# Optimization experiments

Hardware: AMD Instinct MI355X
Metric: run time of the kernel (lower is better)

The kernel has to match this reference:

```python
import jax, jax.numpy as jnp
import numpy as np

# Straight-through binarization: forward hard threshold, backward identity.
# Matches BinarizeTensorThresh / BinarizedLinearFunction / BinaryActivation STE
# semantics from the diffnaps my_layers module (grad_weight = g^T x, i.e. the
# continuous weight receives the gradient of the binary weight unchanged).

def make_ste(thresh):
    @jax.custom_vjp
    def f(x):
        return (x >= thresh).astype(x.dtype)
    def fwd(x):
        return f(x), None
    def bwd(_, g):
        return (g,)
    f.defvjp(fwd, bwd)
    return f

ste_half = make_ste(0.5)  # weight binarization threshold (the 0.5 ctor arg)
ste_one = make_ste(1.0)   # activation fires when (pre-act + bias) >= 1

B, D, H, L = 4096, 5000, 2000, 50  # batch, input_dim(items), hidden_dim(patterns), label_dim
DATA_SPARSITY = 0.05


def setup_inputs() -> dict:
    key = jax.random.key(0)
    k = jax.random.split(key, 5)
    # sparse binary transaction data
    x = (jax.random.uniform(k[0], (B, D)) < DATA_SPARSITY).astype(jnp.float32)
    # continuous encoder weight in [0,1); binarized at 0.5 inside forward
    W_enc = jax.random.uniform(k[1], (H, D), dtype=jnp.float32)
    # small negative encoder bias (BinaPs-style init)
    b_enc = -jnp.abs(jax.random.normal(k[2], (H,), dtype=jnp.float32)) * 0.1
    act0_bias = jnp.zeros((H,), jnp.float32)
    act3_bias = jnp.zeros((D,), jnp.float32)
    # classifier_weight = logit(clip(N(0.1, 0.1), 0.01, 0.99)) as in __init__
    y = jnp.clip(0.1 + 0.1 * jax.random.normal(k[3], (L, H), dtype=jnp.float32), 0.01, 0.99)
    classifier_weight = jnp.log(y / (1.0 - y))
    return {
        "x": x,
        "W_enc": W_enc,
        "b_enc": b_enc,
        "act0_bias": act0_bias,
        "act3_bias": act3_bias,
        "classifier_weight": classifier_weight,
    }


def reference(x, W_enc, b_enc, act0_bias, act3_bias, classifier_weight):
    # fc0_enc: binarized-weight linear with bias
    Wb = ste_half(W_enc)                       # [H, D] in {0,1}
    h = x @ Wb.T + b_enc                       # [B, H]
    # act0: binary activation (threshold 1 on biased pre-activation)
    z = ste_one(h + act0_bias)                 # [B, H]
    # classify: sigmoid-gated classifier head (external_classifier=None / mode 'None')
    final_w = jax.nn.sigmoid(classifier_weight / 0.5)  # [L, H]
    classification = z @ final_w.T             # [B, L]
    # fc3_dec: shares the binarized encoder weight, transposed, no bias
    xd = z @ Wb                                # [B, D]
    output = ste_one(xd + act3_bias)           # [B, D]
    return output, classification, z
```

## Files before the change

### kernel.cpp

```cpp
#include <hip/hip_runtime.h>
#include <stdint.h>

static constexpr int Bn = 4096;
static constexpr int Dn = 5000;
static constexpr int Hn = 2000;
static constexpr int Ln = 50;
static constexpr int XW = 80;
static constexpr int Hpad = 2048;
static constexpr int Dpad = 5120;

typedef int v4i __attribute__((ext_vector_type(4)));
typedef int v16i __attribute__((ext_vector_type(16)));

__device__ __forceinline__ int popc_acc(uint64_t v, int acc) {
  acc = __builtin_popcount((uint32_t)v) + acc;
  acc = __builtin_popcount((uint32_t)(v >> 32)) + acc;
  return acc;
}

__global__ void k_pack_i8(const float* __restrict__ src, uint8_t* __restrict__ dst,
                          int nrows_out, int nrows_valid, int ncols_src) {
  int g = (int)blockIdx.x * 256 + (int)threadIdx.x;
  int row = g / (Dpad / 4);
  int c4 = g - row * (Dpad / 4);
  if (row >= nrows_out) return;
  int col = c4 * 4;
  uchar4 o = make_uchar4(0, 0, 0, 0);
  if (row < nrows_valid && col + 3 < ncols_src) {
    const float4 v = *(const float4*)(src + (size_t)row * ncols_src + col);
    o.x = v.x >= 0.5f; o.y = v.y >= 0.5f; o.z = v.z >= 0.5f; o.w = v.w >= 0.5f;
  }
  *(uchar4*)(dst + (size_t)row * Dpad + col) = o;
}

__global__ void k_pack_x(const float* __restrict__ x, uint64_t* __restrict__ xb2) {
  int g = (int)((blockIdx.x * blockDim.x + threadIdx.x) >> 6);
  int lane = (int)(threadIdx.x & 63);
  constexpr int nq = XW >> 2;
  int row = g / nq;
  int q = g - row * nq;
  if (row >= Bn) return;
  int w0 = q << 2;
  unsigned long long m[4];
#pragma unroll
  for (int e = 0; e < 4; ++e) {
    int col = ((w0 + e) << 6) + lane;
    float v = (col < Dn) ? x[(size_t)row * Dn + col] : 0.0f;
    m[e] = __ballot(v >= 0.5f);
  }
  if (lane < 4) {
    unsigned long long mv = m[0];
    mv = (lane == 1) ? m[1] : mv;
    mv = (lane == 2) ? m[2] : mv;
    mv = (lane == 3) ? m[3] : mv;
    int w = w0 + lane;
    xb2[((size_t)(w >> 1) * Bn + row) * 2 + (w & 1)] = mv;
  }
}

__global__ void k_pack_w(const float* __restrict__ W, uint64_t* __restrict__ wbT) {
  int g = (int)((blockIdx.x * blockDim.x + threadIdx.x) >> 6);
  int lane = (int)(threadIdx.x & 63);
  constexpr int nq = XW >> 2;
  int row = g / nq;
  int q = g - row * nq;
  if (row >= Hn) return;
  int w0 = q << 2;
  unsigned long long m[4];
#pragma unroll
  for (int e = 0; e < 4; ++e) {
    int col = ((w0 + e) << 6) + lane;
    float v = (col < Dn) ? W[(size_t)row * Dn + col] : 0.0f;
    m[e] = __ballot(v >= 0.5f);
  }
  if (lane < 4) {
    unsigned long long mv = m[0];
    mv = (lane == 1) ? m[1] : mv;
    mv = (lane == 2) ? m[2] : mv;
    mv = (lane == 3) ? m[3] : mv;
    wbT[(size_t)(w0 + lane) * Hpad + row] = mv;
  }
}

__global__ void k_transp(const uint64_t* __restrict__ wbT, uint32_t* __restrict__ wt32) {
  int g = (int)((blockIdx.x * blockDim.x + threadIdx.x) >> 6);
  int lane = (int)(threadIdx.x & 63);
  int w = g % XW;
  int jc = g / XW;
  if (jc >= Hpad / 64) return;
  uint64_t word = wbT[(size_t)w * Hpad + jc * 64 + lane];
  uint64_t mym = 0;
#pragma unroll
  for (int e = 0; e < 64; ++e) {
    unsigned long long m = __ballot((word >> e) & 1ull);
    mym = (lane == e) ? m : mym;
  }
  int d = w * 64 + lane;
  wt32[(size_t)(jc * 2) * Dpad + d] = (uint32_t)mym;
  wt32[(size_t)(jc * 2 + 1) * Dpad + d] = (uint32_t)(mym >> 32);
}

__global__ void k_pack_fwT(const float* __restrict__ cw, float* __restrict__ fwT) {
  int idx = blockIdx.x * blockDim.x + threadIdx.x;
  if (idx >= Hn * 64) return;
  int j = idx >> 6, l = idx & 63;
  float v = 0.0f;
  if (l < Ln) {
    float t = 2.0f * cw[(size_t)l * Hn + j];
    v = 1.0f / (1.0f + expf(-t));
  }
  fwT[idx] = v;
}

__global__ void k_zero(float* __restrict__ p, int n) {
  int i = blockIdx.x * blockDim.x + threadIdx.x;
  if (i < n) p[i] = 0.0f;
}

__global__ __launch_bounds__(256) void k_enc_mfma(
    const uint8_t* __restrict__ A,
    const uint8_t* __restrict__ B,
    const float* __restrict__ b_enc, const float* __restrict__ act0b,
    float* __restrict__ z_out, uint32_t* __restrict__ zb32) {
  __shared__ uint8_t As[128 * 128];
  __shared__ uint8_t Bs[128 * 128];
  int tid = (int)threadIdx.x;
  int bn = (int)blockIdx.x;
  int bm = (int)blockIdx.y;
  int wv = __builtin_amdgcn_readfirstlane(tid >> 6);
  int lane = tid & 63;
  int wm = wv >> 1, wn = wv & 1;

  v16i acc[2][2];
#pragma unroll
  for (int i = 0; i < 2; ++i)
#pragma unroll
    for (int j = 0; j < 2; ++j) acc[i][j] = (v16i)0;

  int srow = tid >> 3;
  int sq = tid & 7;
  int ldsw = srow * 128 + ((sq ^ (srow & 7)) << 4);
  const uint8_t* ap = A + ((size_t)(bm * 128 + srow)) * Dpad + sq * 16;
  const uint8_t* bp = B + ((size_t)(bn * 128 + srow)) * Dpad + sq * 16;

  int arow = wm * 64 + (lane & 31);
  int brow = wn * 64 + (lane & 31);
  int khalf = lane >> 5;
  int asw = arow & 7;
  int bsw = brow & 7;

#pragma unroll 1
  for (int kt = 0; kt < 40; ++kt) {
    int k0 = kt * 128;
    v4i ra[4], rb[4];
#pragma unroll
    for (int i = 0; i < 4; ++i) {
      ra[i] = *(const v4i*)(ap + k0 + (size_t)i * 32 * Dpad);
      rb[i] = *(const v4i*)(bp + k0 + (size_t)i * 32 * Dpad);
    }
    __syncthreads();
#pragma unroll
    for (int i = 0; i < 4; ++i) {
      *(v4i*)(As + i * 4096 + ldsw) = ra[i];
      *(v4i*)(Bs + i * 4096 + ldsw) = rb[i];
    }
    __syncthreads();
#pragma unroll
    for (int kk = 0; kk < 4; ++kk) {
      int kq = kk * 2 + khalf;
      v4i a0 = *(const v4i*)(As + arow * 128 + ((kq ^ asw) << 4));
      v4i a1 = *(const v4i*)(As + (arow + 32) * 128 + ((kq ^ asw) << 4));
      v4i b0 = *(const v4i*)(Bs + brow * 128 + ((kq ^ bsw) << 4));
      v4i b1 = *(const v4i*)(Bs + (brow + 32) * 128 + ((kq ^ bsw) << 4));
      acc[0][0] = __builtin_amdgcn_mfma_i32_32x32x32_i8(a0, b0, acc[0][0], 0, 0, 0);
      acc[0][1] = __builtin_amdgcn_mfma_i32_32x32x32_i8(a0, b1, acc[0][1], 0, 0, 0);
      acc[1][0] = __builtin_amdgcn_mfma_i32_32x32x32_i8(a1, b0, acc[1][0], 0, 0, 0);
      acc[1][1] = __builtin_amdgcn_mfma_i32_32x32x32_i8(a1, b1, acc[1][1], 0, 0, 0);
    }
  }

  int col0 = bn * 128 + wn * 64 + (lane & 31);
#pragma unroll
  for (int ni = 0; ni < 2; ++ni) {
    int j = col0 + ni * 32;
    int js = (j < Hn) ? j : (Hn - 1);
    float be = b_enc[js];
    float ab = act0b[js];
    bool jv = j < Hn;
    int hw = (bn * 128 + wn * 64 + ni * 32) >> 5;
#pragma unroll
    for (int mi = 0; mi < 2; ++mi) {
      int rbase = bm * 128 + wm * 64 + mi * 32;
#pragma unroll
      for (int r = 0; r < 16; ++r) {
        int rloc = (r & 3) + 8 * (r >> 2) + 4 * (lane >> 5);
        int b = rbase + rloc;
        float h = ((float)acc[mi][ni][r] + be) + ab;
        bool zb = jv && (h >= 1.0f);
        if (jv) z_out[(size_t)b * Hn + j] = zb ? 1.0f : 0.0f;
        unsigned long long m = __ballot(zb);
        if (lane == 0) {
          int blo = rbase + (r & 3) + 8 * (r >> 2);
          zb32[(size_t)hw * Bn + blo] = (uint32_t)m;
          zb32[(size_t)hw * Bn + blo + 4] = (uint32_t)(m >> 32);
        }
      }
    }
  }
}

__global__ __launch_bounds__(256) void k_enc_bit(const uint64_t* __restrict__ xb2,
                                                 const uint64_t* __restrict__ wbT,
                                                 const float* __restrict__ b_enc,
                                                 const float* __restrict__ act0b,
                                                 float* __restrict__ z_out,
                                                 uint8_t* __restrict__ zb8) {
  __shared__ uint64_t wl[XW][8];
  int tid = (int)threadIdx.x;
  int jg = (int)blockIdx.x;
  int j0 = jg << 3;
#pragma unroll
  for (int k = 0; k < 3; ++k) {
    int idx = k * 256 + tid;
    if (idx < XW * 8) {
      int w = idx >> 3, j = idx & 7;
      wl[w][j] = wbT[(size_t)w * Hpad + j0 + j];
    }
  }
  __syncthreads();
  int wv = __builtin_amdgcn_readfirstlane(tid >> 6);
  int lane = tid & 63;
  int bg = (int)blockIdx.y * 4 + wv;
  int b0 = (bg << 8) + lane;
  int acc[4][8] = {};
  const uint64_t* xp = xb2 + 2 * (size_t)b0;
#pragma unroll 1
  for (int w2 = 0; w2 < XW / 2; ++w2) {
    ulong2 xx[4];
#pragma unroll
    for (int i = 0; i < 4; ++i)
      xx[i] = *(const ulong2*)(xp + ((size_t)w2 * Bn + i * 64) * 2);
#pragma unroll
    for (int t2 = 0; t2 < 4; ++t2) {
      ulong2 wa = *(ulong2*)&wl[2 * w2][2 * t2];
      ulong2 wb = *(ulong2*)&wl[2 * w2 + 1][2 * t2];
#pragma unroll
      for (int i = 0; i < 4; ++i) {
        acc[i][2 * t2]     = popc_acc(xx[i].x & wa.x, acc[i][2 * t2]);
        acc[i][2 * t2 + 1] = popc_acc(xx[i].x & wa.y, acc[i][2 * t2 + 1]);
        acc[i][2 * t2]     = popc_acc(xx[i].y & wb.x, acc[i][2 * t2]);
        acc[i][2 * t2 + 1] = popc_acc(xx[i].y & wb.y, acc[i][2 * t2 + 1]);
      }
    }
  }
  float be[8], ab[8];
#pragma unroll
  for (int t = 0; t < 8; ++t) {
    int j = j0 + t;
    int js = (j < Hn) ? j : (Hn - 1);
    be[t] = b_enc[js];
    ab[t] = act0b[js];
  }
#pragma unroll
  for (int i = 0; i < 4; ++i) {
    int b = b0 + i * 64;
    uint32_t zbyte = 0;
    float zf[8];
#pragma unroll
    for (int t = 0; t < 8; ++t) {
      int j = j0 + t;
      float h = ((float)acc[i][t] + be[t]) + ab[t];
      bool zb = (j < Hn) && (h >= 1.0f);
      zbyte |= zb ? (1u << t) : 0u;
      zf[t] = zb ? 1.0f : 0.0f;
    }
    zb8[((size_t)(jg >> 2) * Bn + b) * 4 + (jg & 3)] = (uint8_t)zbyte;
    if (j0 < Hn) {
      float* zp = z_out + (size_t)b * Hn + j0;
      *(float4*)zp = make_float4(zf[0], zf[1], zf[2], zf[3]);
      *(float4*)(zp + 4) = make_float4(zf[4], zf[5], zf[6], zf[7]);
    }
  }
}

__global__ __launch_bounds__(256, 6) void k_dec(const uint32_t* __restrict__ zb32,
                                                const uint32_t* __restrict__ wt32,
                                                const float* __restrict__ act3b,
                                                float* __restrict__ out) {
  __shared__ uint32_t tl[64][8];
  int tid = (int)threadIdx.x;
  int dc = (int)blockIdx.x;
  int d0 = dc << 3;
  {
#pragma unroll
    for (int k = 0; k < 2; ++k) {
      int e = k * 256 + tid;
      int hw = e >> 3, dl = e & 7;
      tl[hw][dl] = wt32[(size_t)hw * Dpad + d0 + dl];
    }
  }
  __syncthreads();
  int wv = __builtin_amdgcn_readfirstlane(tid >> 6);
  int lane = tid & 63;
  int bg = (int)blockIdx.y * 4 + wv;
  int b0 = (bg << 8) + lane;
  int acc[4][8] = {};
  const uint32_t* zp = zb32 + b0;
  uint32_t z0, z1, z2, z3, n0, n1, n2, n3;
  uint4 wA, wB, wAn, wBn;
  z0 = zp[0]; z1 = zp[64]; z2 = zp[128]; z3 = zp[192];
  wA = *(const uint4*)&tl[0][0];
  wB = *(const uint4*)&tl[0][4];
#define DEC_MAC()                                          \
  do {                                                     \
    acc[0][0] = __builtin_popcount(z0 & wA.x) + acc[0][0]; \
    acc[0][1] = __builtin_popcount(z0 & wA.y) + acc[0][1]; \
    acc[0][2] = __builtin_popcount(z0 & wA.z) + acc[0][2]; \
    acc[0][3] = __builtin_popcount(z0 & wA.w) + acc[0][3]; \
    acc[0][4] = __builtin_popcount(z0 & wB.x) + acc[0][4]; \
    acc[0][5] = __builtin_popcount(z0 & wB.y) + acc[0][5]; \
    acc[0][6] = __builtin_popcount(z0 & wB.z) + acc[0][6]; \
    acc[0][7] = __builtin_popcount(z0 & wB.w) + acc[0][7]; \
    acc[1][0] = __builtin_popcount(z1 & wA.x) + acc[1][0]; \
    acc[1][1] = __builtin_popcount(z1 & wA.y) + acc[1][1]; \
    acc[1][2] = __builtin_popcount(z1 & wA.z) + acc[1][2]; \
    acc[1][3] = __builtin_popcount(z1 & wA.w) + acc[1][3]; \
    acc[1][4] = __builtin_popcount(z1 & wB.x) + acc[1][4]; \
    acc[1][5] = __builtin_popcount(z1 & wB.y) + acc[1][5]; \
    acc[1][6] = __builtin_popcount(z1 & wB.z) + acc[1][6]; \
    acc[1][7] = __builtin_popcount(z1 & wB.w) + acc[1][7]; \
    acc[2][0] = __builtin_popcount(z2 & wA.x) + acc[2][0]; \
    acc[2][1] = __builtin_popcount(z2 & wA.y) + acc[2][1]; \
    acc[2][2] = __builtin_popcount(z2 & wA.z) + acc[2][2]; \
    acc[2][3] = __builtin_popcount(z2 & wA.w) + acc[2][3]; \
    acc[2][4] = __builtin_popcount(z2 & wB.x) + acc[2][4]; \
    acc[2][5] = __builtin_popcount(z2 & wB.y) + acc[2][5]; \
    acc[2][6] = __builtin_popcount(z2 & wB.z) + acc[2][6]; \
    acc[2][7] = __builtin_popcount(z2 & wB.w) + acc[2][7]; \
    acc[3][0] = __builtin_popcount(z3 & wA.x) + acc[3][0]; \
    acc[3][1] = __builtin_popcount(z3 & wA.y) + acc[3][1]; \
    acc[3][2] = __builtin_popcount(z3 & wA.z) + acc[3][2]; \
    acc[3][3] = __builtin_popcount(z3 & wA.w) + acc[3][3]; \
    acc[3][4] = __builtin_popcount(z3 & wB.x) + acc[3][4]; \
    acc[3][5] = __builtin_popcount(z3 & wB.y) + acc[3][5]; \
    acc[3][6] = __builtin_popcount(z3 & wB.z) + acc[3][6]; \
    acc[3][7] = __builtin_popcount(z3 & wB.w) + acc[3][7]; \
  } while (0)
#pragma unroll 1
  for (int hw = 0; hw < 64; ++hw) {
    int hn = (hw < 63) ? hw + 1 : hw;
    const uint32_t* zq = zp + (size_t)hn * Bn;
    n0 = zq[0]; n1 = zq[64]; n2 = zq[128]; n3 = zq[192];
    wAn = *(const uint4*)&tl[hn][0];
    wBn = *(const uint4*)&tl[hn][4];
    DEC_MAC();
    z0 = n0; z1 = n1; z2 = n2; z3 = n3;
    wA = wAn; wB = wBn;
  }
#undef DEC_MAC
  float ab[8];
#pragma unroll
  for (int t = 0; t < 8; ++t) {
    int d = d0 + t;
    int ds = (d < Dn) ? d : (Dn - 1);
    ab[t] = act3b[ds];
  }
  if (d0 < Dn) {
#pragma unroll
    for (int i = 0; i < 4; ++i) {
      int b = b0 + i * 64;
      float of[8];
#pragma unroll
      for (int t = 0; t < 8; ++t)
        of[t] = (((float)acc[i][t] + ab[t]) >= 1.0f) ? 1.0f : 0.0f;
      float* op = out + (size_t)b * Dn + d0;
      *(float4*)op = make_float4(of[0], of[1], of[2], of[3]);
      *(float4*)(op + 4) = make_float4(of[4], of[5], of[6], of[7]);
    }
  }
}

__global__ __launch_bounds__(256) void k_cls(const float* __restrict__ z,
                                             const float* __restrict__ fwT,
                                             float* __restrict__ cls) {
  __shared__ float zT[64][132];
  __shared__ float fwL[64][64];
  int tid = (int)threadIdx.x;
  int bb0 = (int)blockIdx.x * 128;
  int jsp = (int)blockIdx.y;
  int tx = tid & 15, ty = tid >> 4;
  float acc[8][4] = {};
  for (int tile = 0; tile < 4; ++tile) {
    int jt0 = jsp * 256 + tile * 64;
    __syncthreads();
#pragma unroll
    for (int k = 0; k < 8; ++k) {
      int idx = k * 256 + tid;
      int r = idx >> 4, c4 = idx & 15;
      int j = jt0 + c4 * 4;
      float4 v = make_float4(0.f, 0.f, 0.f, 0.f);
      if (j < Hn) v = *(const float4*)(z + (size_t)(bb0 + r) * Hn + j);
      zT[c4 * 4 + 0][r] = v.x;
      zT[c4 * 4 + 1][r] = v.y;
      zT[c4 * 4 + 2][r] = v.z;
      zT[c4 * 4 + 3][r] = v.w;
    }
#pragma unroll
    for (int k = 0; k < 4; ++k) {
      int idx = k * 256 + tid;
      int jj = idx >> 4, c4 = idx & 15;
      int j = jt0 + jj;
      float4 v = make_float4(0.f, 0.f, 0.f, 0.f);
      if (j < Hn) v = *(const float4*)(fwT + (size_t)j * 64 + c4 * 4);
      *(float4*)&fwL[jj][c4 * 4] = v;
    }
    __syncthreads();
#pragma unroll 4
    for (int jj = 0; jj < 64; ++jj) {
      float4 fv = *(float4*)&fwL[jj][tx * 4];
      float4 za = *(float4*)&zT[jj][ty * 8];
      float4 zb = *(float4*)&zT[jj][ty * 8 + 4];
      float zz[8] = {za.x, za.y, za.z, za.w, zb.x, zb.y, zb.z, zb.w};
      float ff[4] = {fv.x, fv.y, fv.z, fv.w};
#pragma unroll
      for (int i = 0; i < 8; ++i)
#pragma unroll
        for (int l = 0; l < 4; ++l) acc[i][l] += zz[i] * ff[l];
    }
  }
#pragma unroll
  for (int i = 0; i < 8; ++i) {
    int b = bb0 + ty * 8 + i;
#pragma unroll
    for (int l = 0; l < 4; ++l) {
      int L = tx * 4 + l;
      if (L < Ln) atomicAdd(&cls[(size_t)b * Ln + L], acc[i][l]);
    }
  }
}

extern "C" void kernel_launch(void* const* d_in, const int* in_sizes, int n_in,
                              void* d_out, int out_size, void* d_ws, size_t ws_size,
                              hipStream_t stream) {
  const float* x     = (const float*)d_in[0];
  const float* W     = (const float*)d_in[1];
  const float* b_enc = (const float*)d_in[2];
  const float* act0b = (const float*)d_in[3];
  const float* act3b = (const float*)d_in[4];
  const float* cw    = (const float*)d_in[5];

  float* out0 = (float*)d_out;
  float* cls  = out0 + (size_t)Bn * Dn;
  float* zout = cls + (size_t)Bn * Ln;

  char* ws = (char*)d_ws;
  uint64_t* wbT  = (uint64_t*)ws; ws += (size_t)XW * Hpad * 8;
  uint32_t* wt32 = (uint32_t*)ws; ws += (size_t)64 * Dpad * 4;
  uint32_t* zb32 = (uint32_t*)ws; ws += (size_t)64 * Bn * 4;
  float*    fwT  = (float*)ws;    ws += (size_t)Hn * 64 * 4;
  size_t common = (size_t)(ws - (char*)d_ws);
  size_t need_mfma = common + (size_t)Bn * Dpad + (size_t)Hpad * Dpad;
  size_t need_bit = common + (size_t)XW * Bn * 8;

  {
    long long waves = (long long)Hn * (XW / 4);
    k_pack_w<<<(int)((waves * 64 + 255) / 256), 256, 0, stream>>>(W, wbT);
  }
  {
    long long waves = (long long)(Hpad / 64) * XW;
    k_transp<<<(int)((waves * 64 + 255) / 256), 256, 0, stream>>>(wbT, wt32);
  }
  k_pack_fwT<<<(Hn * 64 + 255) / 256, 256, 0, stream>>>(cw, fwT);
  k_zero<<<(Bn * Ln + 255) / 256, 256, 0, stream>>>(cls, Bn * Ln);

  if (ws_size >= need_mfma) {
    uint8_t* xi8 = (uint8_t*)ws;
    uint8_t* wi8 = xi8 + (size_t)Bn * Dpad;
    k_pack_i8<<<(Bn * (Dpad / 4) + 255) / 256, 256, 0, stream>>>(x, xi8, Bn, Bn, Dn);
    k_pack_i8<<<(Hpad * (Dpad / 4) + 255) / 256, 256, 0, stream>>>(W, wi8, Hpad, Hn, Dn);
    dim3 ge(Hpad / 128, Bn / 128);
    k_enc_mfma<<<ge, 256, 0, stream>>>(xi8, wi8, b_enc, act0b, zout, zb32);
  } else {
    uint64_t* xb2 = (uint64_t*)ws;
    {
      long long waves = (long long)Bn * (XW / 4);
      k_pack_x<<<(int)((waves * 64 + 255) / 256), 256, 0, stream>>>(x, xb2);
    }
    (void)need_bit;
    dim3 g1(256, 4);
    k_enc_bit<<<g1, 256, 0, stream>>>(xb2, wbT, b_enc, act0b, zout, (uint8_t*)zb32);
  }

  dim3 g3(32, 8);
  k_cls<<<g3, 256, 0, stream>>>(zout, fwT, cls);

  dim3 g2(640, 4);
  k_dec<<<g2, 256, 0, stream>>>(zb32, wt32, act3b, out0);
}
```

Baseline: 248.9 us.

## Compute decoder with int8 MFMA using byte z and transposed weight buffers

```diff
diff --git a/kernel.cpp b/kernel.cpp
--- a/kernel.cpp
+++ b/kernel.cpp
@@ -33,6 +33,34 @@
   *(uchar4*)(dst + (size_t)row * Dpad + col) = o;
 }
 
+__global__ __launch_bounds__(256) void k_pack_w_dual(const float* __restrict__ W,
+                                                     uint8_t* __restrict__ wi8,
+                                                     uint8_t* __restrict__ wtd) {
+  int d = (int)blockIdx.x * 256 + (int)threadIdx.x;
+  int j0 = (int)blockIdx.y * 64;
+  bool dv = d < Dn;
+  uint64_t colbits = 0;
+  for (int r = 0; r < 64; ++r) {
+    int j = j0 + r;
+    float v = (j < Hn && dv) ? W[(size_t)j * Dn + d] : 0.0f;
+    uint8_t bit = (v >= 0.5f) ? 1 : 0;
+    wi8[(size_t)j * Dpad + d] = bit;
+    colbits |= ((uint64_t)bit) << r;
+  }
+  uint8_t* dst = wtd + (size_t)d * Hpad + j0;
+#pragma unroll
+  for (int q = 0; q < 4; ++q) {
+    uint32_t u[4];
+#pragma unroll
+    for (int s = 0; s < 4; ++s) {
+      uint32_t nib = (uint32_t)((colbits >> (q * 16 + s * 4)) & 0xFull);
+      u[s] = (nib & 1u) | (((nib >> 1) & 1u) << 8) | (((nib >> 2) & 1u) << 16) |
+             (((nib >> 3) & 1u) << 24);
+    }
+    *(uint4*)(dst + q * 16) = make_uint4(u[0], u[1], u[2], u[3]);
+  }
+}
+
 __global__ void k_pack_x(const float* __restrict__ x, uint64_t* __restrict__ xb2) {
   int g = (int)((blockIdx.x * blockDim.x + threadIdx.x) >> 6);
   int lane = (int)(threadIdx.x & 63);
@@ -118,10 +146,10 @@
 }
 
 __global__ __launch_bounds__(256) void k_enc_mfma(
-    const uint8_t* __restrict__ A,
-    const uint8_t* __restrict__ B,
+    const uint8_t* __restrict__ A, const uint8_t* __restrict__ B,
     const float* __restrict__ b_enc, const float* __restrict__ act0b,
-    float* __restrict__ z_out, uint32_t* __restrict__ zb32) {
+    float* __restrict__ z_out, uint32_t* __restrict__ zb32,
+    uint8_t* __restrict__ zi8) {
   __shared__ uint8_t As[128 * 128];
   __shared__ uint8_t Bs[128 * 128];
   int tid = (int)threadIdx.x;
@@ -197,13 +225,97 @@
         int b = rbase + rloc;
         float h = ((float)acc[mi][ni][r] + be) + ab;
         bool zb = jv && (h >= 1.0f);
-        if (jv) z_out[(size_t)b * Hn + j] = zb ? 1.0f : 0.0f;
+        if (jv) {
+          z_out[(size_t)b * Hn + j] = zb ? 1.0f : 0.0f;
+          if (zi8) zi8[(size_t)b * Hpad + j] = zb ? 1 : 0;
+        }
         unsigned long long m = __ballot(zb);
         if (lane == 0) {
           int blo = rbase + (r & 3) + 8 * (r >> 2);
           zb32[(size_t)hw * Bn + blo] = (uint32_t)m;
           zb32[(size_t)hw * Bn + blo + 4] = (uint32_t)(m >> 32);
         }
+      }
+    }
+  }
+}
+
+__global__ __launch_bounds__(256) void k_dec_mfma(
+    const uint8_t* __restrict__ A,
+    const uint8_t* __restrict__ B,
+    const float* __restrict__ act3b, float* __restrict__ out) {
+  __shared__ uint8_t As[128 * 128];
+  __shared__ uint8_t Bs[128 * 128];
+  int tid = (int)threadIdx.x;
+  int bn = (int)blockIdx.x;
+  int bm = (int)blockIdx.y;
+  int wv = __builtin_amdgcn_readfirstlane(tid >> 6);
+  int lane = tid & 63;
+  int wm = wv >> 1, wn = wv & 1;
+
+  v16i acc[2][2];
+#pragma unroll
+  for (int i = 0; i < 2; ++i)
+#pragma unroll
+    for (int j = 0; j < 2; ++j) acc[i][j] = (v16i)0;
+
+  int srow = tid >> 3;
+  int sq = tid & 7;
+  int ldsw = srow * 128 + ((sq ^ (srow & 7)) << 4);
+  const uint8_t* ap = A + ((size_t)(bm * 128 + srow)) * Hpad + sq * 16;
+  const uint8_t* bp = B + ((size_t)(bn * 128 + srow)) * Hpad + sq * 16;
+
+  int arow = wm * 64 + (lane & 31);
+  int brow = wn * 64 + (lane & 31);
+  int khalf = lane >> 5;
+  int asw = arow & 7;
+  int bsw = brow & 7;
+
+#pragma unroll 1
+  for (int kt = 0; kt < 16; ++kt) {
+    int k0 = kt * 128;
+    v4i ra[4], rb[4];
+#pragma unroll
+    for (int i = 0; i < 4; ++i) {
+      ra[i] = *(const v4i*)(ap + k0 + (size_t)i * 32 * Hpad);
+      rb[i] = *(const v4i*)(bp + k0 + (size_t)i * 32 * Hpad);
+    }
+    __syncthreads();
+#pragma unroll
+    for (int i = 0; i < 4; ++i) {
+      *(v4i*)(As + i * 4096 + ldsw) = ra[i];
+      *(v4i*)(Bs + i * 4096 + ldsw) = rb[i];
+    }
+    __syncthreads();
+#pragma unroll
+    for (int kk = 0; kk < 4; ++kk) {
+      int kq = kk * 2 + khalf;
+      v4i a0 = *(const v4i*)(As + arow * 128 + ((kq ^ asw) << 4));
+      v4i a1 = *(const v4i*)(As + (arow + 32) * 128 + ((kq ^ asw) << 4));
+      v4i b0 = *(const v4i*)(Bs + brow * 128 + ((kq ^ bsw) << 4));
+      v4i b1 = *(const v4i*)(Bs + (brow + 32) * 128 + ((kq ^ bsw) << 4));
+      acc[0][0] = __builtin_amdgcn_mfma_i32_32x32x32_i8(a0, b0, acc[0][0], 0, 0, 0);
+      acc[0][1] = __builtin_amdgcn_mfma_i32_32x32x32_i8(a0, b1, acc[0][1], 0, 0, 0);
+      acc[1][0] = __builtin_amdgcn_mfma_i32_32x32x32_i8(a1, b0, acc[1][0], 0, 0, 0);
+      acc[1][1] = __builtin_amdgcn_mfma_i32_32x32x32_i8(a1, b1, acc[1][1], 0, 0, 0);
+    }
+  }
+
+  int col0 = bn * 128 + wn * 64 + (lane & 31);
+#pragma unroll
+  for (int ni = 0; ni < 2; ++ni) {
+    int d = col0 + ni * 32;
+    int ds = (d < Dn) ? d : (Dn - 1);
+    float ab = act3b[ds];
+    bool dv = d < Dn;
+#pragma unroll
+    for (int mi = 0; mi < 2; ++mi) {
+      int rbase = bm * 128 + wm * 64 + mi * 32;
+#pragma unroll
+      for (int r = 0; r < 16; ++r) {
+        int rloc = (r & 3) + 8 * (r >> 2) + 4 * (lane >> 5);
+        int b = rbase + rloc;
+        if (dv) out[(size_t)b * Dn + d] = (((float)acc[mi][ni][r] + ab) >= 1.0f) ? 1.0f : 0.0f;
       }
     }
   }
@@ -283,10 +395,10 @@
   }
 }
 
-__global__ __launch_bounds__(256, 6) void k_dec(const uint32_t* __restrict__ zb32,
-                                                const uint32_t* __restrict__ wt32,
-                                                const float* __restrict__ act3b,
-                                                float* __restrict__ out) {
+__global__ __launch_bounds__(256, 6) void k_dec_bit(const uint32_t* __restrict__ zb32,
+                                                    const uint32_t* __restrict__ wt32,
+                                                    const float* __restrict__ act3b,
+                                                    float* __restrict__ out) {
   __shared__ uint32_t tl[64][8];
   int tid = (int)threadIdx.x;
   int dc = (int)blockIdx.x;
@@ -380,9 +492,9 @@
   }
 }
 
-__global__ __launch_bounds__(256) void k_cls(const float* __restrict__ z,
-                                             const float* __restrict__ fwT,
-                                             float* __restrict__ cls) {
+__global__ __launch_bounds__(256) void k_cls_i8(const uint8_t* __restrict__ zi8,
+                                                const float* __restrict__ fwT,
+                                                float* __restrict__ cls) {
   __shared__ float zT[64][132];
   __shared__ float fwL[64][64];
   int tid = (int)threadIdx.x;
@@ -398,6 +510,65 @@
       int idx = k * 256 + tid;
       int r = idx >> 4, c4 = idx & 15;
       int j = jt0 + c4 * 4;
+      uchar4 v = make_uchar4(0, 0, 0, 0);
+      if (j < Hn) v = *(const uchar4*)(zi8 + (size_t)(bb0 + r) * Hpad + j);
+      zT[c4 * 4 + 0][r] = (float)v.x;
+      zT[c4 * 4 + 1][r] = (float)v.y;
+      zT[c4 * 4 + 2][r] = (float)v.z;
+      zT[c4 * 4 + 3][r] = (float)v.w;
+    }
+#pragma unroll
+    for (int k = 0; k < 4; ++k) {
+      int idx = k * 256 + tid;
+      int jj = idx >> 4, c4 = idx & 15;
+      int j = jt0 + jj;
+      float4 v = make_float4(0.f, 0.f, 0.f, 0.f);
+      if (j < Hn) v = *(const float4*)(fwT + (size_t)j * 64 + c4 * 4);
+      *(float4*)&fwL[jj][c4 * 4] = v;
+    }
+    __syncthreads();
+#pragma unroll 4
+    for (int jj = 0; jj < 64; ++jj) {
+      float4 fv = *(float4*)&fwL[jj][tx * 4];
+      float4 za = *(float4*)&zT[jj][ty * 8];
+      float4 zb = *(float4*)&zT[jj][ty * 8 + 4];
+      float zz[8] = {za.x, za.y, za.z, za.w, zb.x, zb.y, zb.z, zb.w};
+      float ff[4] = {fv.x, fv.y, fv.z, fv.w};
+#pragma unroll
+      for (int i = 0; i < 8; ++i)
+#pragma unroll
+        for (int l = 0; l < 4; ++l) acc[i][l] += zz[i] * ff[l];
+    }
+  }
+#pragma unroll
+  for (int i = 0; i < 8; ++i) {
+    int b = bb0 + ty * 8 + i;
+#pragma unroll
+    for (int l = 0; l < 4; ++l) {
+      int L = tx * 4 + l;
+      if (L < Ln) atomicAdd(&cls[(size_t)b * Ln + L], acc[i][l]);
+    }
+  }
+}
+
+__global__ __launch_bounds__(256) void k_cls_f32(const float* __restrict__ z,
+                                                 const float* __restrict__ fwT,
+                                                 float* __restrict__ cls) {
+  __shared__ float zT[64][132];
+  __shared__ float fwL[64][64];
+  int tid = (int)threadIdx.x;
+  int bb0 = (int)blockIdx.x * 128;
+  int jsp = (int)blockIdx.y;
+  int tx = tid & 15, ty = tid >> 4;
+  float acc[8][4] = {};
+  for (int tile = 0; tile < 4; ++tile) {
+    int jt0 = jsp * 256 + tile * 64;
+    __syncthreads();
+#pragma unroll
+    for (int k = 0; k < 8; ++k) {
+      int idx = k * 256 + tid;
+      int r = idx >> 4, c4 = idx & 15;
+      int j = jt0 + c4 * 4;
       float4 v = make_float4(0.f, 0.f, 0.f, 0.f);
       if (j < Hn) v = *(const float4*)(z + (size_t)(bb0 + r) * Hn + j);
       zT[c4 * 4 + 0][r] = v.x;
@@ -453,47 +624,79 @@
   float* cls  = out0 + (size_t)Bn * Dn;
   float* zout = cls + (size_t)Bn * Ln;
 
-  char* ws = (char*)d_ws;
-  uint64_t* wbT  = (uint64_t*)ws; ws += (size_t)XW * Hpad * 8;
-  uint32_t* wt32 = (uint32_t*)ws; ws += (size_t)64 * Dpad * 4;
-  uint32_t* zb32 = (uint32_t*)ws; ws += (size_t)64 * Bn * 4;
-  float*    fwT  = (float*)ws;    ws += (size_t)Hn * 64 * 4;
-  size_t common = (size_t)(ws - (char*)d_ws);
-  size_t need_mfma = common + (size_t)Bn * Dpad + (size_t)Hpad * Dpad;
-  size_t need_bit = common + (size_t)XW * Bn * 8;
-
-  {
-    long long waves = (long long)Hn * (XW / 4);
-    k_pack_w<<<(int)((waves * 64 + 255) / 256), 256, 0, stream>>>(W, wbT);
-  }
-  {
-    long long waves = (long long)(Hpad / 64) * XW;
-    k_transp<<<(int)((waves * 64 + 255) / 256), 256, 0, stream>>>(wbT, wt32);
-  }
+  char* p = (char*)d_ws;
+  uint32_t* zb32 = (uint32_t*)p; p += (size_t)64 * Bn * 4;
+  float*    fwT  = (float*)p;    p += (size_t)Hn * 64 * 4;
+  size_t common = (size_t)(p - (char*)d_ws);
+
+  size_t sz_xi8 = (size_t)Bn * Dpad;
+  size_t sz_wi8 = (size_t)Hpad * Dpad;
+  size_t sz_zi8 = (size_t)Bn * Hpad;
+  size_t sz_wtd = (size_t)Dpad * Hpad;
+  size_t sz_wbT = (size_t)XW * Hpad * 8;
+  size_t sz_wt32 = (size_t)64 * Dpad * 4;
+  size_t full_need = common + sz_xi8 + sz_wi8 + sz_zi8 + sz_wtd;
+  size_t mid_need  = common + sz_wbT + sz_wt32 + sz_xi8 + sz_wi8;
+
   k_pack_fwT<<<(Hn * 64 + 255) / 256, 256, 0, stream>>>(cw, fwT);
   k_zero<<<(Bn * Ln + 255) / 256, 256, 0, stream>>>(cls, Bn * Ln);
 
-  if (ws_size >= need_mfma) {
-    uint8_t* xi8 = (uint8_t*)ws;
-    uint8_t* wi8 = xi8 + (size_t)Bn * Dpad;
+  if (ws_size >= full_need) {
+    uint8_t* xi8 = (uint8_t*)p;
+    uint8_t* wi8 = xi8 + sz_xi8;
+    uint8_t* zi8 = wi8 + sz_wi8;
+    uint8_t* wtd = zi8 + sz_zi8;
+    k_pack_i8<<<(Bn * (Dpad / 4) + 255) / 256, 256, 0, stream>>>(x, xi8, Bn, Bn, Dn);
+    dim3 gwd(Dpad / 256, Hpad / 64);
+    k_pack_w_dual<<<gwd, 256, 0, stream>>>(W, wi8, wtd);
+    dim3 ge(Hpad / 128, Bn / 128);
+    k_enc_mfma<<<ge, 256, 0, stream>>>(xi8, wi8, b_enc, act0b, zout, zb32, zi8);
+    dim3 g3(32, 8);
+    k_cls_i8<<<g3, 256, 0, stream>>>(zi8, fwT, cls);
+    dim3 gd(Dpad / 128, Bn / 128);
+    k_dec_mfma<<<gd, 256, 0, stream>>>(zi8, wtd, act3b, out0);
+  } else if (ws_size >= mid_need) {
+    uint64_t* wbT  = (uint64_t*)p;
+    uint32_t* wt32 = (uint32_t*)(p + sz_wbT);
+    uint8_t*  xi8  = (uint8_t*)(p + sz_wbT + sz_wt32);
+    uint8_t*  wi8  = xi8 + sz_xi8;
+    {
+      long long waves = (long long)Hn * (XW / 4);
+      k_pack_w<<<(int)((waves * 64 + 255) / 256), 256, 0, stream>>>(W, wbT);
+    }
+    {
+      long long waves = (long long)(Hpad / 64) * XW;
+      k_transp<<<(int)((waves * 64 + 255) / 256), 256, 0, stream>>>(wbT, wt32);
+    }
     k_pack_i8<<<(Bn * (Dpad / 4) + 255) / 256, 256, 0, stream>>>(x, xi8, Bn, Bn, Dn);
     k_pack_i8<<<(Hpad * (Dpad / 4) + 255) / 256, 256, 0, stream>>>(W, wi8, Hpad, Hn, Dn);
     dim3 ge(Hpad / 128, Bn / 128);
-    k_enc_mfma<<<ge, 256, 0, stream>>>(xi8, wi8, b_enc, act0b, zout, zb32);
+    k_enc_mfma<<<ge, 256, 0, stream>>>(xi8, wi8, b_enc, act0b, zout, zb32, (uint8_t*)nullptr);
+    dim3 g3(32, 8);
+    k_cls_f32<<<g3, 256, 0, stream>>>(zout, fwT, cls);
+    dim3 g2(640, 4);
+    k_dec_bit<<<g2, 256, 0, stream>>>(zb32, wt32, act3b, out0);
   } else {
-    uint64_t* xb2 = (uint64_t*)ws;
+    uint64_t* wbT  = (uint64_t*)p;
+    uint32_t* wt32 = (uint32_t*)(p + sz_wbT);
+    uint64_t* xb2  = (uint64_t*)(p + sz_wbT + sz_wt32);
+    {
+      long long waves = (long long)Hn * (XW / 4);
+      k_pack_w<<<(int)((waves * 64 + 255) / 256), 256, 0, stream>>>(W, wbT);
+    }
+    {
+      long long waves = (long long)(Hpad / 64) * XW;
+      k_transp<<<(int)((waves * 64 + 255) / 256), 256, 0, stream>>>(wbT, wt32);
+    }
     {
       long long waves = (long long)Bn * (XW / 4);
       k_pack_x<<<(int)((waves * 64 + 255) / 256), 256, 0, stream>>>(x, xb2);
     }
-    (void)need_bit;
     dim3 g1(256, 4);
     k_enc_bit<<<g1, 256, 0, stream>>>(xb2, wbT, b_enc, act0b, zout, (uint8_t*)zb32);
-  }
-
-  dim3 g3(32, 8);
-  k_cls<<<g3, 256, 0, stream>>>(zout, fwT, cls);
-
-  dim3 g2(640, 4);
-  k_dec<<<g2, 256, 0, stream>>>(zb32, wt32, act3b, out0);
-}
+    dim3 g3(32, 8);
+    k_cls_f32<<<g3, 256, 0, stream>>>(zout, fwT, cls);
+    dim3 g2(640, 4);
+    k_dec_bit<<<g2, 256, 0, stream>>>(zb32, wt32, act3b, out0);
+  }
+}
```

Result: faster. 238.2 us (-4.3%).
